# Kernel tuning notes

Measured on AMD Instinct MI355X. Metric: run time of the kernel, lower is better.

## Reference

```python
import jax, jax.numpy as jnp
import numpy as np

B, T, C = 4, 2048, 1024
N_HEAD = 16
HEAD_DIM = C // N_HEAD


def setup_inputs() -> dict:
    key = jax.random.key(0)
    ks = jax.random.split(key, 5)
    scale = 0.02
    return {
        "x": jax.random.normal(ks[0], (B, T, C), dtype=jnp.float32),
        "w_attn": jax.random.normal(ks[1], (C, 3 * C), dtype=jnp.float32) * scale,
        "b_attn": jax.random.normal(ks[2], (3 * C,), dtype=jnp.float32) * scale,
        "w_proj": jax.random.normal(ks[3], (C, C), dtype=jnp.float32) * scale,
        "b_proj": jax.random.normal(ks[4], (C,), dtype=jnp.float32) * scale,
    }


def reference(x, w_attn, b_attn, w_proj, b_proj):
    Bq, Tq, Cq = x.shape
    qkv = x @ w_attn + b_attn  # [B, T, 3C]
    q, k, v = jnp.split(qkv, 3, axis=2)
    # [B, H, T, D]
    q = q.reshape(Bq, Tq, N_HEAD, HEAD_DIM).transpose(0, 2, 1, 3)
    k = k.reshape(Bq, Tq, N_HEAD, HEAD_DIM).transpose(0, 2, 1, 3)
    v = v.reshape(Bq, Tq, N_HEAD, HEAD_DIM).transpose(0, 2, 1, 3)
    att = jnp.einsum("bhqd,bhkd->bhqk", q, k) * (HEAD_DIM ** -0.5)
    causal = jnp.tril(jnp.ones((Tq, Tq), dtype=bool))
    att = jnp.where(causal[None, None, :, :], att, -jnp.inf)
    att = jax.nn.softmax(att, axis=-1)
    out = jnp.einsum("bhqk,bhkd->bhqd", att, v)  # [B, H, T, D]
    out = out.transpose(0, 2, 1, 3).reshape(Bq, Tq, Cq)
    return out @ w_proj + b_proj
```

## Files before the change

kernel.cpp:

```cpp
#include <hip/hip_runtime.h>
#include <hip/hip_bf16.h>

#define Bsz 4
#define Tsz 2048
#define Csz 1024
#define NH  16
#define HD  64
#define NT  (Bsz * Tsz)

typedef unsigned short u16;
typedef unsigned int   u32;
typedef u16   u16x8  __attribute__((ext_vector_type(8)));
typedef u16   u16x4  __attribute__((ext_vector_type(4)));
typedef u32   u32x2  __attribute__((ext_vector_type(2)));
typedef short s16x8  __attribute__((ext_vector_type(8)));
typedef float f32x4  __attribute__((ext_vector_type(4)));

__device__ __forceinline__ float b2f(u16 u) {
    union { unsigned int i; float f; } x; x.i = ((unsigned int)u) << 16; return x.f;
}
__device__ __forceinline__ u16 f2b(float f) {
    unsigned int u = __float_as_uint(f);
    return (u16)((u + 0x7FFF + ((u >> 16) & 1)) >> 16);
}
__device__ __forceinline__ float ex2(float x) {
    float r; asm("v_exp_f32 %0, %1" : "=v"(r) : "v"(x)); return r;
}
__device__ __forceinline__ u32 cvtpk(float lo, float hi) {
    u32 r; asm("v_cvt_pk_bf16_f32 %0, %1, %2" : "=v"(r) : "v"(lo), "v"(hi)); return r;
}
__device__ __forceinline__ void gload16(const u16* g, u16* l) {
    __builtin_amdgcn_global_load_lds(
        (const __attribute__((address_space(1))) void*)g,
        (__attribute__((address_space(3))) void*)l, 16, 0, 0);
}
__device__ __forceinline__ void tr4(u32 a, u16x4 t[4]) {
    asm volatile("ds_read_b64_tr_b16 %0, %1"             : "=v"(t[0]) : "v"(a));
    asm volatile("ds_read_b64_tr_b16 %0, %1 offset:512"  : "=v"(t[1]) : "v"(a));
    asm volatile("ds_read_b64_tr_b16 %0, %1 offset:1024" : "=v"(t[2]) : "v"(a));
    asm volatile("ds_read_b64_tr_b16 %0, %1 offset:1536" : "=v"(t[3]) : "v"(a));
}
#define LGKM0_FENCE() do { \
    asm volatile("s_waitcnt lgkmcnt(0)" ::: "memory"); \
    __builtin_amdgcn_sched_barrier(0); } while (0)

__global__ __launch_bounds__(256)
void conv_f32_bf16(const float* __restrict__ in, u16* __restrict__ out, int n8)
{
    int t = blockIdx.x * 256 + threadIdx.x;
    if (t >= n8) return;
    const float4* p = reinterpret_cast<const float4*>(in) + (size_t)t * 2;
    float4 a = p[0], b = p[1];
    u16x8 w;
    w[0] = f2b(a.x); w[1] = f2b(a.y); w[2] = f2b(a.z); w[3] = f2b(a.w);
    w[4] = f2b(b.x); w[5] = f2b(b.y); w[6] = f2b(b.z); w[7] = f2b(b.w);
    *(reinterpret_cast<u16x8*>(out) + t) = w;
}

__global__ __launch_bounds__(256)
void transpose_conv(const float* __restrict__ in, u16* __restrict__ out, int K, int N)
{
    __shared__ float tile[32][33];
    const int n0 = blockIdx.x * 32, k0 = blockIdx.y * 32;
    const int tx = threadIdx.x & 31, ty = threadIdx.x >> 5;
#pragma unroll
    for (int j = 0; j < 4; ++j)
        tile[ty + j * 8][tx] = in[(size_t)(k0 + ty + j * 8) * N + n0 + tx];
    __syncthreads();
#pragma unroll
    for (int j = 0; j < 4; ++j)
        out[(size_t)(n0 + ty + j * 8) * K + k0 + tx] = f2b(tile[tx][ty + j * 8]);
}

template<typename OutT>
__global__ __launch_bounds__(256)
void gemm_bf16(const u16* __restrict__ A, const u16* __restrict__ Bt,
               const float* __restrict__ bias, OutT* __restrict__ C,
               int M, int N, int K)
{
    __shared__ u16 As[128 * 64];
    __shared__ u16 Bs[128 * 64];

    const int tid  = threadIdx.x;
    const int lane = tid & 63;
    const int wid  = tid >> 6;
    const int wr   = wid >> 1;
    const int wc   = wid & 1;
    const int g    = lane >> 4;
    const int rr   = lane & 15;
    const int srow = lane >> 3;
    const int sslt = lane & 7;

    const int n0 = blockIdx.x * 128;
    const int m0 = blockIdx.y * 128;

    f32x4 acc[4][4];
#pragma unroll
    for (int m = 0; m < 4; ++m)
#pragma unroll
        for (int n = 0; n < 4; ++n) acc[m][n] = (f32x4){0.f, 0.f, 0.f, 0.f};

    for (int k0 = 0; k0 < K; k0 += 64) {
        __syncthreads();
#pragma unroll
        for (int p = 0; p < 4; ++p) {
            const int q = p * 4 + wid;
            const int r = q * 8 + srow;
            gload16(A  + (size_t)(m0 + r) * K + k0 + sslt * 8, &As[q * 512]);
            gload16(Bt + (size_t)(n0 + r) * K + k0 + sslt * 8, &Bs[q * 512]);
        }
        __syncthreads();

#pragma unroll
        for (int kk = 0; kk < 2; ++kk) {
            s16x8 af[4], bfr[4];
            const int s = kk * 4 + g;
#pragma unroll
            for (int m = 0; m < 4; ++m)
                af[m] = *reinterpret_cast<const s16x8*>(
                    &As[(wr * 64 + m * 16 + rr) * 64 + s * 8]);
#pragma unroll
            for (int n = 0; n < 4; ++n)
                bfr[n] = *reinterpret_cast<const s16x8*>(
                    &Bs[(wc * 64 + n * 16 + rr) * 64 + s * 8]);
#pragma unroll
            for (int m = 0; m < 4; ++m)
#pragma unroll
                for (int n = 0; n < 4; ++n)
                    acc[m][n] = __builtin_amdgcn_mfma_f32_16x16x32_bf16(
                        af[m], bfr[n], acc[m][n], 0, 0, 0);
        }
    }

#pragma unroll
    for (int m = 0; m < 4; ++m) {
#pragma unroll
        for (int n = 0; n < 4; ++n) {
            const int col = n0 + wc * 64 + n * 16 + rr;
            const float bv = bias[col];
#pragma unroll
            for (int j = 0; j < 4; ++j) {
                const int row = m0 + wr * 64 + m * 16 + g * 4 + j;
                const float v = acc[m][n][j] + bv;
                if constexpr (sizeof(OutT) == 2)
                    C[(size_t)row * N + col] = (OutT)f2b(v);
                else
                    C[(size_t)row * N + col] = (OutT)v;
            }
        }
    }
}

__global__ __launch_bounds__(256)
void attn_mfma(const u16* __restrict__ qkv, u16* __restrict__ out)
{
    __shared__ __align__(128) u16 Ks[64 * 64];
    __shared__ __align__(128) u16 Vt[64 * 64];
    __shared__ __align__(128) u16 Pl[4 * 1024];

    const int tid  = threadIdx.x;
    const int lane = tid & 63;
    const int wid  = tid >> 6;
    const int c    = lane & 15;
    const int g    = lane >> 4;

    const int bh = blockIdx.x;
    const int b  = bh >> 4;
    const int h  = bh & 15;

    const int skey = tid >> 3;
    const int sb   = tid & 7;
    const int kswz = (sb ^ (skey & 7)) * 8;
    const int slotc = ((c >> 2) & 1) * 16 + (c >> 3) * 4 + (c & 3);
    const u32 pbyte = ((u32)(size_t)(&Pl[0])) + wid * 2048 + lane * 8;
    const float QSC = 0.18033688f;

    for (int half = 0; half < 2; ++half) {
        const int yt  = half ? 31 - (int)blockIdx.y : (int)blockIdx.y;
        const int t0  = yt * 64;
        const int qb0 = t0 + wid * 16;

        s16x8 qf[2];
#pragma unroll
        for (int kk = 0; kk < 2; ++kk) {
            u16x8 raw = *reinterpret_cast<const u16x8*>(
                qkv + (size_t)(b * Tsz + qb0 + c) * (3 * Csz) + h * HD + kk * 32 + g * 8);
            s16x8 qv;
#pragma unroll
            for (int i = 0; i < 8; ++i) qv[i] = (short)f2b(b2f(raw[i]) * QSC);
            qf[kk] = qv;
        }

        f32x4 acco[4];
#pragma unroll
        for (int dn = 0; dn < 4; ++dn) acco[dn] = (f32x4){0.f, 0.f, 0.f, 0.f};
        float mrun[4], lrun[4];
#pragma unroll
        for (int i = 0; i < 4; ++i) { mrun[i] = -1e30f; lrun[i] = 0.f; }

        for (int kt = 0; kt <= t0; kt += 64) {
            __syncthreads();
#pragma unroll
            for (int p = 0; p < 2; ++p) {
                const int key = skey + p * 32;
                const u16* gk = qkv + (size_t)(b * Tsz + kt + key) * (3 * Csz)
                                + Csz + h * HD + sb * 8;
                u16x8 kv = *reinterpret_cast<const u16x8*>(gk);
                u16x8 vv = *reinterpret_cast<const u16x8*>(gk + Csz);
                *reinterpret_cast<u16x8*>(&Ks[key * 64 + kswz]) = kv;
#pragma unroll
                for (int i = 0; i < 8; ++i) {
                    const int d = sb * 8 + i;
                    Vt[d * 64 + (key ^ (((i ^ sb) & 7) << 3))] = vv[i];
                }
            }
            __syncthreads();

            f32x4 accS[4];
#pragma unroll
            for (int n = 0; n < 4; ++n) accS[n] = (f32x4){0.f, 0.f, 0.f, 0.f};
            __builtin_amdgcn_s_setprio(1);
#pragma unroll
            for (int kk = 0; kk < 2; ++kk) {
                s16x8 kf[4];
#pragma unroll
                for (int n = 0; n < 4; ++n) {
                    const int key = n * 16 + c;
                    kf[n] = *reinterpret_cast<const s16x8*>(
                        &Ks[key * 64 + (((kk * 4 + g) ^ (c & 7)) * 8)]);
                }
#pragma unroll
                for (int n = 0; n < 4; ++n)
                    accS[n] = __builtin_amdgcn_mfma_f32_16x16x32_bf16(
                        qf[kk], kf[n], accS[n], 0, 0, 0);
            }
            __builtin_amdgcn_s_setprio(0);

            if (kt == t0) {
#pragma unroll
                for (int n = 0; n < 4; ++n) {
                    const int kgl = kt + n * 16 + c;
#pragma unroll
                    for (int j = 0; j < 4; ++j)
                        if (kgl > qb0 + g * 4 + j) accS[n][j] = -1e30f;
                }
            }

            float pm[4];
#pragma unroll
            for (int j = 0; j < 4; ++j)
                pm[j] = fmaxf(fmaxf(accS[0][j], accS[1][j]),
                              fmaxf(accS[2][j], accS[3][j]));
#pragma unroll
            for (int msk = 1; msk < 16; msk <<= 1)
#pragma unroll
                for (int i = 0; i < 4; ++i)
                    pm[i] = fmaxf(pm[i], __shfl_xor(pm[i], msk));

            int need = 0;
#pragma unroll
            for (int i = 0; i < 4; ++i) need |= (pm[i] > mrun[i] + 8.f);
            if (__any(need)) {
                float cv[4];
#pragma unroll
                for (int i = 0; i < 4; ++i) {
                    const float mn = fmaxf(mrun[i], pm[i]);
                    cv[i] = ex2(mrun[i] - mn);
                    mrun[i] = mn;
                    lrun[i] *= cv[i];
                }
#pragma unroll
                for (int dn = 0; dn < 4; ++dn)
#pragma unroll
                    for (int j = 0; j < 4; ++j)
                        acco[dn][j] *= cv[j];
            }

#pragma unroll
            for (int n = 0; n < 4; ++n) {
                float pv[4];
#pragma unroll
                for (int j = 0; j < 4; ++j) {
                    pv[j] = ex2(accS[n][j] - mrun[j]);
                    lrun[j] += pv[j];
                }
                const int slot = (n >> 1) * 32 + (n & 1) * 8 + slotc;
                *reinterpret_cast<u32x2*>(&Pl[wid * 1024 + slot * 16 + g * 4]) =
                    (u32x2){cvtpk(pv[0], pv[1]), cvtpk(pv[2], pv[3])};
            }
            LGKM0_FENCE();

            u16x4 tp[4];
            tr4(pbyte, tp);
            LGKM0_FENCE();
            s16x8 pa[2];
#pragma unroll
            for (int kk = 0; kk < 2; ++kk)
#pragma unroll
                for (int q = 0; q < 4; ++q) {
                    pa[kk][q]     = (short)tp[kk * 2][q];
                    pa[kk][q + 4] = (short)tp[kk * 2 + 1][q];
                }

#pragma unroll
            for (int kk = 0; kk < 2; ++kk) {
                s16x8 vf[4];
#pragma unroll
                for (int dn = 0; dn < 4; ++dn) {
                    const int d = dn * 16 + c;
                    const int swz = (c & 7) ^ ((dn * 2 + (c >> 3)) & 7);
                    vf[dn] = *reinterpret_cast<const s16x8*>(
                        &Vt[d * 64 + (((kk * 4 + g) ^ swz) * 8)]);
                }
                __builtin_amdgcn_s_setprio(1);
#pragma unroll
                for (int dn = 0; dn < 4; ++dn)
                    acco[dn] = __builtin_amdgcn_mfma_f32_16x16x32_bf16(
                        pa[kk], vf[dn], acco[dn], 0, 0, 0);
                __builtin_amdgcn_s_setprio(0);
            }
        }

#pragma unroll
        for (int msk = 1; msk < 16; msk <<= 1)
#pragma unroll
            for (int i = 0; i < 4; ++i)
                lrun[i] += __shfl_xor(lrun[i], msk);
        float inv[4];
#pragma unroll
        for (int i = 0; i < 4; ++i) inv[i] = 1.f / lrun[i];
#pragma unroll
        for (int dn = 0; dn < 4; ++dn)
#pragma unroll
            for (int j = 0; j < 4; ++j) {
                const int q = qb0 + g * 4 + j;
                out[(size_t)(b * Tsz + q) * Csz + h * HD + dn * 16 + c] =
                    f2b(acco[dn][j] * inv[j]);
            }
    }
}

extern "C" void kernel_launch(void* const* d_in, const int* in_sizes, int n_in,
                              void* d_out, int out_size, void* d_ws, size_t ws_size,
                              hipStream_t stream) {
    const float* x      = (const float*)d_in[0];
    const float* w_attn = (const float*)d_in[1];
    const float* b_attn = (const float*)d_in[2];
    const float* w_proj = (const float*)d_in[3];
    const float* b_proj = (const float*)d_in[4];
    float* out = (float*)d_out;

    char* w = (char*)d_ws;
    u16* qkv_bf = (u16*)w;  w += (size_t)NT * 3 * Csz * 2;
    u16* x_bf   = (u16*)w;  w += (size_t)NT * Csz * 2;
    u16* ao_bf  = (u16*)w;  w += (size_t)NT * Csz * 2;
    u16* wat    = (u16*)w;  w += (size_t)3 * Csz * Csz * 2;
    u16* wpt    = (u16*)w;

    conv_f32_bf16<<<(NT * Csz / 8 + 255) / 256, 256, 0, stream>>>(x, x_bf, NT * Csz / 8);
    transpose_conv<<<dim3(3 * Csz / 32, Csz / 32), 256, 0, stream>>>(w_attn, wat, Csz, 3 * Csz);
    transpose_conv<<<dim3(Csz / 32, Csz / 32), 256, 0, stream>>>(w_proj, wpt, Csz, Csz);

    gemm_bf16<u16><<<dim3(3 * Csz / 128, NT / 128), 256, 0, stream>>>(
        x_bf, wat, b_attn, qkv_bf, NT, 3 * Csz, Csz);

    attn_mfma<<<dim3(Bsz * NH, 16), 256, 0, stream>>>(qkv_bf, ao_bf);

    gemm_bf16<float><<<dim3(Csz / 128, NT / 128), 256, 0, stream>>>(
        ao_bf, wpt, b_proj, out, NT, Csz, Csz);
}
```

Baseline: 316.1 us.

## Compute transposed scores to keep P in registers and double-buffer K/V tiles

The attention kernel now computes S^T (K·Q) so that each lane holds one query column. This lets the softmax probabilities be packed straight into the MFMA A-operand layout, with V columns permuted to match, removing the LDS round-trip and transposed reads for P. K/V tiles are double-buffered in shared memory, and the next tile's global loads are issued before the compute on the current one, which drops one barrier per iteration. The row max and sum now use fewer shuffles but need extra shuffles to broadcast the rescale factors. Launch bounds are set to 4 blocks per CU, which may limit registers.

```diff
diff --git a/kernel.cpp b/kernel.cpp
--- a/kernel.cpp
+++ b/kernel.cpp
@@ -11,8 +11,6 @@
 typedef unsigned short u16;
 typedef unsigned int   u32;
 typedef u16   u16x8  __attribute__((ext_vector_type(8)));
-typedef u16   u16x4  __attribute__((ext_vector_type(4)));
-typedef u32   u32x2  __attribute__((ext_vector_type(2)));
 typedef short s16x8  __attribute__((ext_vector_type(8)));
 typedef float f32x4  __attribute__((ext_vector_type(4)));
 
@@ -34,15 +32,6 @@
         (const __attribute__((address_space(1))) void*)g,
         (__attribute__((address_space(3))) void*)l, 16, 0, 0);
 }
-__device__ __forceinline__ void tr4(u32 a, u16x4 t[4]) {
-    asm volatile("ds_read_b64_tr_b16 %0, %1"             : "=v"(t[0]) : "v"(a));
-    asm volatile("ds_read_b64_tr_b16 %0, %1 offset:512"  : "=v"(t[1]) : "v"(a));
-    asm volatile("ds_read_b64_tr_b16 %0, %1 offset:1024" : "=v"(t[2]) : "v"(a));
-    asm volatile("ds_read_b64_tr_b16 %0, %1 offset:1536" : "=v"(t[3]) : "v"(a));
-}
-#define LGKM0_FENCE() do { \
-    asm volatile("s_waitcnt lgkmcnt(0)" ::: "memory"); \
-    __builtin_amdgcn_sched_barrier(0); } while (0)
 
 __global__ __launch_bounds__(256)
 void conv_f32_bf16(const float* __restrict__ in, u16* __restrict__ out, int n8)
@@ -151,12 +140,11 @@
     }
 }
 
-__global__ __launch_bounds__(256)
+__global__ __launch_bounds__(256, 4)
 void attn_mfma(const u16* __restrict__ qkv, u16* __restrict__ out)
 {
-    __shared__ __align__(128) u16 Ks[64 * 64];
-    __shared__ __align__(128) u16 Vt[64 * 64];
-    __shared__ __align__(128) u16 Pl[4 * 1024];
+    __shared__ __align__(128) u16 Ks[2][64 * 64];
+    __shared__ __align__(128) u16 Vt[2][64 * 64];
 
     const int tid  = threadIdx.x;
     const int lane = tid & 63;
@@ -171,9 +159,24 @@
     const int skey = tid >> 3;
     const int sb   = tid & 7;
     const int kswz = (sb ^ (skey & 7)) * 8;
-    const int slotc = ((c >> 2) & 1) * 16 + (c >> 3) * 4 + (c & 3);
-    const u32 pbyte = ((u32)(size_t)(&Pl[0])) + wid * 2048 + lane * 8;
+    const int vswz = ((c & 7) ^ ((0 * 2 + (c >> 3)) & 7));
     const float QSC = 0.18033688f;
+
+    auto vcol = [](int s) {
+        return (s & 32) | (((s >> 3) & 1) << 4) | (((s >> 2) & 1) << 3)
+             | (((s >> 4) & 1) << 2) | (s & 3);
+    };
+
+    u16x8 kreg[2], vreg[2];
+    const u16* kvbase = qkv + (size_t)b * Tsz * (3 * Csz) + Csz + h * HD + sb * 8;
+    auto load_kv = [&](int kt) {
+#pragma unroll
+        for (int p = 0; p < 2; ++p) {
+            const u16* gk = kvbase + (size_t)(kt + skey + p * 32) * (3 * Csz);
+            kreg[p] = *reinterpret_cast<const u16x8*>(gk);
+            vreg[p] = *reinterpret_cast<const u16x8*>(gk + Csz);
+        }
+    };
 
     for (int half = 0; half < 2; ++half) {
         const int yt  = half ? 31 - (int)blockIdx.y : (int)blockIdx.y;
@@ -194,31 +197,29 @@
         f32x4 acco[4];
 #pragma unroll
         for (int dn = 0; dn < 4; ++dn) acco[dn] = (f32x4){0.f, 0.f, 0.f, 0.f};
-        float mrun[4], lrun[4];
-#pragma unroll
-        for (int i = 0; i < 4; ++i) { mrun[i] = -1e30f; lrun[i] = 0.f; }
+        float mrun = -1e30f, lrun = 0.f;
+
+        load_kv(0);
 
         for (int kt = 0; kt <= t0; kt += 64) {
-            __syncthreads();
+            const int bi = (kt >> 6) & 1;
 #pragma unroll
             for (int p = 0; p < 2; ++p) {
                 const int key = skey + p * 32;
-                const u16* gk = qkv + (size_t)(b * Tsz + kt + key) * (3 * Csz)
-                                + Csz + h * HD + sb * 8;
-                u16x8 kv = *reinterpret_cast<const u16x8*>(gk);
-                u16x8 vv = *reinterpret_cast<const u16x8*>(gk + Csz);
-                *reinterpret_cast<u16x8*>(&Ks[key * 64 + kswz]) = kv;
+                *reinterpret_cast<u16x8*>(&Ks[bi][key * 64 + kswz]) = kreg[p];
+                const int vc = vcol(key);
 #pragma unroll
                 for (int i = 0; i < 8; ++i) {
                     const int d = sb * 8 + i;
-                    Vt[d * 64 + (key ^ (((i ^ sb) & 7) << 3))] = vv[i];
+                    Vt[bi][d * 64 + (vc ^ (((i ^ sb) & 7) << 3))] = vreg[p][i];
                 }
             }
+            if (kt < t0) load_kv(kt + 64);
             __syncthreads();
 
-            f32x4 accS[4];
-#pragma unroll
-            for (int n = 0; n < 4; ++n) accS[n] = (f32x4){0.f, 0.f, 0.f, 0.f};
+            f32x4 accT[4];
+#pragma unroll
+            for (int n = 0; n < 4; ++n) accT[n] = (f32x4){0.f, 0.f, 0.f, 0.f};
             __builtin_amdgcn_s_setprio(1);
 #pragma unroll
             for (int kk = 0; kk < 2; ++kk) {
@@ -227,80 +228,56 @@
                 for (int n = 0; n < 4; ++n) {
                     const int key = n * 16 + c;
                     kf[n] = *reinterpret_cast<const s16x8*>(
-                        &Ks[key * 64 + (((kk * 4 + g) ^ (c & 7)) * 8)]);
+                        &Ks[bi][key * 64 + (((kk * 4 + g) ^ (c & 7)) * 8)]);
                 }
 #pragma unroll
                 for (int n = 0; n < 4; ++n)
-                    accS[n] = __builtin_amdgcn_mfma_f32_16x16x32_bf16(
-                        qf[kk], kf[n], accS[n], 0, 0, 0);
+                    accT[n] = __builtin_amdgcn_mfma_f32_16x16x32_bf16(
+                        kf[n], qf[kk], accT[n], 0, 0, 0);
             }
             __builtin_amdgcn_s_setprio(0);
 
             if (kt == t0) {
 #pragma unroll
-                for (int n = 0; n < 4; ++n) {
-                    const int kgl = kt + n * 16 + c;
+                for (int n = 0; n < 4; ++n)
 #pragma unroll
                     for (int j = 0; j < 4; ++j)
-                        if (kgl > qb0 + g * 4 + j) accS[n][j] = -1e30f;
-                }
-            }
-
-            float pm[4];
-#pragma unroll
-            for (int j = 0; j < 4; ++j)
-                pm[j] = fmaxf(fmaxf(accS[0][j], accS[1][j]),
-                              fmaxf(accS[2][j], accS[3][j]));
-#pragma unroll
-            for (int msk = 1; msk < 16; msk <<= 1)
-#pragma unroll
-                for (int i = 0; i < 4; ++i)
-                    pm[i] = fmaxf(pm[i], __shfl_xor(pm[i], msk));
-
-            int need = 0;
-#pragma unroll
-            for (int i = 0; i < 4; ++i) need |= (pm[i] > mrun[i] + 8.f);
-            if (__any(need)) {
-                float cv[4];
-#pragma unroll
-                for (int i = 0; i < 4; ++i) {
-                    const float mn = fmaxf(mrun[i], pm[i]);
-                    cv[i] = ex2(mrun[i] - mn);
-                    mrun[i] = mn;
-                    lrun[i] *= cv[i];
-                }
+                        if (kt + n * 16 + g * 4 + j > qb0 + c) accT[n][j] = -1e30f;
+            }
+
+            float pm = accT[0][0];
+#pragma unroll
+            for (int n = 0; n < 4; ++n)
+#pragma unroll
+                for (int j = 0; j < 4; ++j) pm = fmaxf(pm, accT[n][j]);
+            pm = fmaxf(pm, __shfl_xor(pm, 16));
+            pm = fmaxf(pm, __shfl_xor(pm, 32));
+
+            if (__any(pm > mrun + 8.f)) {
+                const float mn = fmaxf(mrun, pm);
+                const float cv = ex2(mrun - mn);
+                mrun = mn;
+                lrun *= cv;
+                float cvo[4];
+#pragma unroll
+                for (int j = 0; j < 4; ++j) cvo[j] = __shfl(cv, g * 4 + j);
 #pragma unroll
                 for (int dn = 0; dn < 4; ++dn)
 #pragma unroll
-                    for (int j = 0; j < 4; ++j)
-                        acco[dn][j] *= cv[j];
-            }
-
+                    for (int j = 0; j < 4; ++j) acco[dn][j] *= cvo[j];
+            }
+
+            union { u32 w[8]; s16x8 frag[2]; } pu;
 #pragma unroll
             for (int n = 0; n < 4; ++n) {
-                float pv[4];
-#pragma unroll
-                for (int j = 0; j < 4; ++j) {
-                    pv[j] = ex2(accS[n][j] - mrun[j]);
-                    lrun[j] += pv[j];
-                }
-                const int slot = (n >> 1) * 32 + (n & 1) * 8 + slotc;
-                *reinterpret_cast<u32x2*>(&Pl[wid * 1024 + slot * 16 + g * 4]) =
-                    (u32x2){cvtpk(pv[0], pv[1]), cvtpk(pv[2], pv[3])};
-            }
-            LGKM0_FENCE();
-
-            u16x4 tp[4];
-            tr4(pbyte, tp);
-            LGKM0_FENCE();
-            s16x8 pa[2];
-#pragma unroll
-            for (int kk = 0; kk < 2; ++kk)
-#pragma unroll
-                for (int q = 0; q < 4; ++q) {
-                    pa[kk][q]     = (short)tp[kk * 2][q];
-                    pa[kk][q + 4] = (short)tp[kk * 2 + 1][q];
-                }
+                const float p0 = ex2(accT[n][0] - mrun);
+                const float p1 = ex2(accT[n][1] - mrun);
+                const float p2 = ex2(accT[n][2] - mrun);
+                const float p3 = ex2(accT[n][3] - mrun);
+                lrun += (p0 + p1) + (p2 + p3);
+                pu.w[n * 2]     = cvtpk(p0, p1);
+                pu.w[n * 2 + 1] = cvtpk(p2, p3);
+            }
 
 #pragma unroll
             for (int kk = 0; kk < 2; ++kk) {
@@ -310,34 +287,34 @@
                     const int d = dn * 16 + c;
                     const int swz = (c & 7) ^ ((dn * 2 + (c >> 3)) & 7);
                     vf[dn] = *reinterpret_cast<const s16x8*>(
-                        &Vt[d * 64 + (((kk * 4 + g) ^ swz) * 8)]);
+                        &Vt[bi][d * 64 + (((kk * 4 + g) ^ swz) * 8)]);
                 }
                 __builtin_amdgcn_s_setprio(1);
 #pragma unroll
                 for (int dn = 0; dn < 4; ++dn)
                     acco[dn] = __builtin_amdgcn_mfma_f32_16x16x32_bf16(
-                        pa[kk], vf[dn], acco[dn], 0, 0, 0);
+                        pu.frag[kk], vf[dn], acco[dn], 0, 0, 0);
                 __builtin_amdgcn_s_setprio(0);
             }
         }
 
-#pragma unroll
-        for (int msk = 1; msk < 16; msk <<= 1)
-#pragma unroll
-            for (int i = 0; i < 4; ++i)
-                lrun[i] += __shfl_xor(lrun[i], msk);
-        float inv[4];
-#pragma unroll
-        for (int i = 0; i < 4; ++i) inv[i] = 1.f / lrun[i];
+        lrun += __shfl_xor(lrun, 16);
+        lrun += __shfl_xor(lrun, 32);
+        const float inv = 1.f / lrun;
+        float invo[4];
+#pragma unroll
+        for (int j = 0; j < 4; ++j) invo[j] = __shfl(inv, g * 4 + j);
 #pragma unroll
         for (int dn = 0; dn < 4; ++dn)
 #pragma unroll
             for (int j = 0; j < 4; ++j) {
                 const int q = qb0 + g * 4 + j;
                 out[(size_t)(b * Tsz + q) * Csz + h * HD + dn * 16 + c] =
-                    f2b(acco[dn][j] * inv[j]);
-            }
+                    f2b(acco[dn][j] * invo[j]);
+            }
+        __syncthreads();
     }
+    (void)vswz;
 }
 
 extern "C" void kernel_launch(void* const* d_in, const int* in_sizes, int n_in,
```

After: 273.6 us. 1.16x faster.
